# Performance work log

Measured on AMD Instinct MI355X. Metric: run time of the kernel, lower is better.

The kernel has to match this reference:

```python
import jax, jax.numpy as jnp
import numpy as np

WEIGHT_CE = 1.0
WEIGHT_DICE = 1.0
EPS = 1e-10
SMOOTH = 1e-5


def setup_inputs() -> dict:
    key = jax.random.key(0)
    k1, k2 = jax.random.split(key)
    B, N, H, W, D = 2, 8, 128, 128, 128
    logits = jax.random.normal(k1, (B, N, H, W, D), dtype=jnp.float32)
    pred = jax.nn.softmax(logits, axis=1)  # module expects softmaxed preds
    target = jax.random.randint(k2, (B, 1, H, W, D), 0, N, dtype=jnp.int32)
    return {"pred": pred, "target": target}


def reference(pred, target):
    # pred: (B, N, H, W, D) softmax probs; target: (B, 1, H, W, D) int labels
    B, N = pred.shape[0], pred.shape[1]
    t = target[:, 0]  # (B, H, W, D)

    # --- CE part (faithful to the original's cross-batch one-hot bug) ---
    # loss[b2, hwd] = -sum_b sum_c 1[t[b2,hwd]==c] * log(pred[b,c,hwd]+eps)
    logp_sum = jnp.sum(jnp.log(pred + EPS), axis=0)  # (N, H, W, D)
    gathered = jnp.take_along_axis(
        jnp.broadcast_to(logp_sum[None], (B,) + logp_sum.shape),
        t[:, None], axis=1)[:, 0]  # (B, H, W, D)
    celoss = -jnp.mean(gathered) / B

    # --- MONAI DiceLoss(softmax=False, to_onehot_y=True), defaults ---
    oh = (t[:, None] == jnp.arange(N, dtype=t.dtype)[None, :, None, None, None]).astype(pred.dtype)  # (B,N,H,W,D)
    inter = jnp.sum(oh * pred, axis=(2, 3, 4))   # (B, N)
    ground_o = jnp.sum(oh, axis=(2, 3, 4))       # (B, N)
    pred_o = jnp.sum(pred, axis=(2, 3, 4))       # (B, N)
    dice = jnp.mean(1.0 - (2.0 * inter + SMOOTH) / (ground_o + pred_o + SMOOTH))

    return WEIGHT_CE * celoss + WEIGHT_DICE * dice
```

## Files before the change

### kernel.cpp

```cpp
#include <hip/hip_runtime.h>

#define S_VOX (128*128*128)
#define QV (S_VOX/4)
#define SEGS 256
#define SEG_Q (QV / SEGS)
#define EPSF 1e-10f
#define SMOOTHF 1e-5f

#define NREP 8
#define REP_STRIDE 64
#define CODES_OFF 4096

__device__ __forceinline__ float wave_reduce(float v) {
#pragma unroll
    for (int off = 32; off > 0; off >>= 1)
        v += __shfl_down(v, off, 64);
    return v;
}

__global__ __launch_bounds__(256) void encode_tgt(const int* __restrict__ tgt,
                                                  unsigned char* __restrict__ codes) {
    const int idx = blockIdx.x * 256 + threadIdx.x;
    const int4 a = ((const int4*)tgt)[idx];
    const int4 b = ((const int4*)tgt)[QV + idx];
    uchar4 c;
    c.x = (unsigned char)(a.x | (b.x << 3));
    c.y = (unsigned char)(a.y | (b.y << 3));
    c.z = (unsigned char)(a.z | (b.z << 3));
    c.w = (unsigned char)(a.w | (b.w << 3));
    ((uchar4*)codes)[idx] = c;
}

__global__ __launch_bounds__(256) void dice_main(const float* __restrict__ pred,
                                                 const unsigned char* __restrict__ codes,
                                                 float* __restrict__ ws) {
    const int xcd   = blockIdx.x & 7;
    const int r     = blockIdx.x >> 3;
    const int n     = r & 7;
    const int seg   = ((r >> 3) << 3) | xcd;

    const size_t base = (size_t)seg * SEG_Q;
    const float4* p0 = (const float4*)pred + (size_t)n       * QV + base;
    const float4* p1 = (const float4*)pred + (size_t)(8 + n) * QV + base;
    const uchar4* cd = (const uchar4*)codes + base;

    float ce = 0.f, in0 = 0.f, in1 = 0.f, po0 = 0.f, po1 = 0.f;
    int   g0 = 0, g1 = 0;

    const int i0 = threadIdx.x;

#define LD(q0_, q1_, c_, k)                                             \
    { q0_ = p0[i0 + (k) * 256]; q1_ = p1[i0 + (k) * 256]; c_ = cd[i0 + (k) * 256]; }

#define VOX(pa, pb, cc)                                                 \
    {                                                                   \
        const int m0 = (((cc) & 7) == n);                               \
        const int m1 = ((((cc) >> 3) & 7) == n);                        \
        in0 += m0 ? (pa) : 0.f;  g0 += m0;                              \
        in1 += m1 ? (pb) : 0.f;  g1 += m1;                              \
        ce  += (float)(m0 + m1) * __logf(((pa) + EPSF) * ((pb) + EPSF)); \
        po0 += (pa);  po1 += (pb);                                      \
    }
#define CONS(q0_, q1_, c_)                                              \
    {                                                                   \
        VOX(q0_.x, q1_.x, c_.x)                                         \
        VOX(q0_.y, q1_.y, c_.y)                                         \
        VOX(q0_.z, q1_.z, c_.z)                                         \
        VOX(q0_.w, q1_.w, c_.w)                                         \
    }
#define SB __builtin_amdgcn_sched_barrier(0)

    float4 a0, a1, b0, b1, c0, c1;
    uchar4 ac, bc, cc;
    LD(a0, a1, ac, 0)
    LD(b0, b1, bc, 1)
    SB;
    LD(c0, c1, cc, 2) SB; CONS(a0, a1, ac)
    LD(a0, a1, ac, 3) SB; CONS(b0, b1, bc)
    LD(b0, b1, bc, 4) SB; CONS(c0, c1, cc)
    LD(c0, c1, cc, 5) SB; CONS(a0, a1, ac)
    LD(a0, a1, ac, 6) SB; CONS(b0, b1, bc)
    LD(b0, b1, bc, 7) SB; CONS(c0, c1, cc)
    CONS(a0, a1, ac)
    CONS(b0, b1, bc)
#undef SB
#undef CONS
#undef VOX
#undef LD

    __shared__ float red[4][7];
    const int lane = threadIdx.x & 63;
    const int wave = threadIdx.x >> 6;
    float acc[7] = { ce, in0, in1, (float)g0, (float)g1, po0, po1 };
#pragma unroll
    for (int k = 0; k < 7; k++) {
        float v = wave_reduce(acc[k]);
        if (lane == 0) red[wave][k] = v;
    }
    __syncthreads();
    if (threadIdx.x < 7) {
        const int k = threadIdx.x;
        const float s = red[0][k] + red[1][k] + red[2][k] + red[3][k];
        static const int off[7] = { 0, 1, 9, 17, 25, 33, 41 };
        const int dst = (k == 0) ? 0 : off[k] + n;
        atomicAdd(&ws[xcd * REP_STRIDE + dst], s);
    }
}

__global__ void dice_finalize(const float* __restrict__ ws, float* __restrict__ out) {
    const int i = threadIdx.x;
    float term = 0.f;
    if (i < 16) {
        float inter = 0.f, g = 0.f, p = 0.f;
#pragma unroll
        for (int rp = 0; rp < NREP; rp++) {
            inter += ws[rp * REP_STRIDE + 1  + i];
            g     += ws[rp * REP_STRIDE + 17 + i];
            p     += ws[rp * REP_STRIDE + 33 + i];
        }
        term = 1.0f - (2.0f * inter + SMOOTHF) / (g + p + SMOOTHF);
    }
    term = wave_reduce(term);
    if (i == 0) {
        float ce = 0.f;
#pragma unroll
        for (int rp = 0; rp < NREP; rp++) ce += ws[rp * REP_STRIDE];
        float celoss = -ce / (4.0f * (float)S_VOX);
        out[0] = celoss + term * (1.0f / 16.0f);
    }
}

extern "C" void kernel_launch(void* const* d_in, const int* in_sizes, int n_in,
                              void* d_out, int out_size, void* d_ws, size_t ws_size,
                              hipStream_t stream) {
    const float* pred = (const float*)d_in[0];
    const int*   tgt  = (const int*)d_in[1];
    float* ws  = (float*)d_ws;
    float* out = (float*)d_out;
    unsigned char* codes = (unsigned char*)(ws + CODES_OFF);

    hipMemsetAsync(ws, 0, NREP * REP_STRIDE * sizeof(float), stream);
    encode_tgt<<<QV / 256, 256, 0, stream>>>(tgt, codes);
    dice_main<<<8 * SEGS, 256, 0, stream>>>(pred, codes, ws);
    dice_finalize<<<1, 64, 0, stream>>>(ws, out);
}
```

Baseline: 216.5 us.

## Shrink segments to 4 loads per thread, issue all loads upfront with nontemporal hints

Halves the segment size so each thread handles 4 float4 pairs instead of 8, which doubles the grid. All loads are issued up front instead of being software-pipelined across three register buffers. Pred loads use nontemporal loads to avoid polluting the cache on streaming data. The destination offset table is also replaced by arithmetic. This aims for more memory-level parallelism and occupancy, at the cost of twice as many blocks and twice as many atomics.

```diff
diff --git a/kernel.cpp b/kernel.cpp
--- a/kernel.cpp
+++ b/kernel.cpp
@@ -2,14 +2,16 @@
 
 #define S_VOX (128*128*128)
 #define QV (S_VOX/4)
-#define SEGS 256
-#define SEG_Q (QV / SEGS)
+#define SEG_Q 1024
+#define SEGS (QV / SEG_Q)
 #define EPSF 1e-10f
 #define SMOOTHF 1e-5f
 
 #define NREP 8
 #define REP_STRIDE 64
 #define CODES_OFF 4096
+
+typedef float vf4 __attribute__((ext_vector_type(4)));
 
 __device__ __forceinline__ float wave_reduce(float v) {
 #pragma unroll
@@ -40,8 +42,8 @@
     const int seg   = ((r >> 3) << 3) | xcd;
 
     const size_t base = (size_t)seg * SEG_Q;
-    const float4* p0 = (const float4*)pred + (size_t)n       * QV + base;
-    const float4* p1 = (const float4*)pred + (size_t)(8 + n) * QV + base;
+    const vf4*    p0 = (const vf4*)pred + (size_t)n       * QV + base;
+    const vf4*    p1 = (const vf4*)pred + (size_t)(8 + n) * QV + base;
     const uchar4* cd = (const uchar4*)codes + base;
 
     float ce = 0.f, in0 = 0.f, in1 = 0.f, po0 = 0.f, po1 = 0.f;
@@ -49,44 +51,34 @@
 
     const int i0 = threadIdx.x;
 
-#define LD(q0_, q1_, c_, k)                                             \
-    { q0_ = p0[i0 + (k) * 256]; q1_ = p1[i0 + (k) * 256]; c_ = cd[i0 + (k) * 256]; }
+    vf4 A[4], B[4];
+    uchar4 C[4];
+#pragma unroll
+    for (int k = 0; k < 4; k++) {
+        const int i = i0 + k * 256;
+        A[k] = __builtin_nontemporal_load(&p0[i]);
+        B[k] = __builtin_nontemporal_load(&p1[i]);
+        C[k] = cd[i];
+    }
+    __builtin_amdgcn_sched_barrier(0);
 
-#define VOX(pa, pb, cc)                                                 \
-    {                                                                   \
-        const int m0 = (((cc) & 7) == n);                               \
-        const int m1 = ((((cc) >> 3) & 7) == n);                        \
-        in0 += m0 ? (pa) : 0.f;  g0 += m0;                              \
-        in1 += m1 ? (pb) : 0.f;  g1 += m1;                              \
+#define VOX(pa, pb, cc)                                                  \
+    {                                                                    \
+        const int m0 = (((cc) & 7) == n);                                \
+        const int m1 = ((((cc) >> 3) & 7) == n);                         \
+        in0 += m0 ? (pa) : 0.f;  g0 += m0;                               \
+        in1 += m1 ? (pb) : 0.f;  g1 += m1;                               \
         ce  += (float)(m0 + m1) * __logf(((pa) + EPSF) * ((pb) + EPSF)); \
-        po0 += (pa);  po1 += (pb);                                      \
+        po0 += (pa);  po1 += (pb);                                       \
     }
-#define CONS(q0_, q1_, c_)                                              \
-    {                                                                   \
-        VOX(q0_.x, q1_.x, c_.x)                                         \
-        VOX(q0_.y, q1_.y, c_.y)                                         \
-        VOX(q0_.z, q1_.z, c_.z)                                         \
-        VOX(q0_.w, q1_.w, c_.w)                                         \
+#pragma unroll
+    for (int k = 0; k < 4; k++) {
+        VOX(A[k].x, B[k].x, C[k].x)
+        VOX(A[k].y, B[k].y, C[k].y)
+        VOX(A[k].z, B[k].z, C[k].z)
+        VOX(A[k].w, B[k].w, C[k].w)
     }
-#define SB __builtin_amdgcn_sched_barrier(0)
-
-    float4 a0, a1, b0, b1, c0, c1;
-    uchar4 ac, bc, cc;
-    LD(a0, a1, ac, 0)
-    LD(b0, b1, bc, 1)
-    SB;
-    LD(c0, c1, cc, 2) SB; CONS(a0, a1, ac)
-    LD(a0, a1, ac, 3) SB; CONS(b0, b1, bc)
-    LD(b0, b1, bc, 4) SB; CONS(c0, c1, cc)
-    LD(c0, c1, cc, 5) SB; CONS(a0, a1, ac)
-    LD(a0, a1, ac, 6) SB; CONS(b0, b1, bc)
-    LD(b0, b1, bc, 7) SB; CONS(c0, c1, cc)
-    CONS(a0, a1, ac)
-    CONS(b0, b1, bc)
-#undef SB
-#undef CONS
 #undef VOX
-#undef LD
 
     __shared__ float red[4][7];
     const int lane = threadIdx.x & 63;
@@ -101,8 +93,11 @@
     if (threadIdx.x < 7) {
         const int k = threadIdx.x;
         const float s = red[0][k] + red[1][k] + red[2][k] + red[3][k];
-        static const int off[7] = { 0, 1, 9, 17, 25, 33, 41 };
-        const int dst = (k == 0) ? 0 : off[k] + n;
+        int dst;
+        if (k == 0)      dst = 0;
+        else if (k <= 2) dst = 1  + (k - 1) * 8 + n;
+        else if (k <= 4) dst = 17 + (k - 3) * 8 + n;
+        else             dst = 33 + (k - 5) * 8 + n;
         atomicAdd(&ws[xcd * REP_STRIDE + dst], s);
     }
 }
@@ -139,7 +134,7 @@
     float* out = (float*)d_out;
     unsigned char* codes = (unsigned char*)(ws + CODES_OFF);
 
-    hipMemsetAsync(ws, 0, NREP * REP_STRIDE * sizeof(float), stream);
+    (void)hipMemsetAsync(ws, 0, NREP * REP_STRIDE * sizeof(float), stream);
     encode_tgt<<<QV / 256, 256, 0, stream>>>(tgt, codes);
     dice_main<<<8 * SEGS, 256, 0, stream>>>(pred, codes, ws);
     dice_finalize<<<1, 64, 0, stream>>>(ws, out);
```

Result: faster. 197.9 us (-8.6%).
